# Kernel tuning notes

Measured on AMD Instinct MI355X. Metric: run time of the kernel, lower is better.

## Reference

```python
import jax, jax.numpy as jnp
import numpy as np

BATCH, SEQ = 1, 2048
D_MODEL, N_HEADS, D_HEAD = 2048, 16, 128
ROTARY_DIM = 128
N_CTX = 2048
EPS = 1e-5
IGNORE = -100000.0
ATTN_SCALE = float(np.sqrt(D_HEAD))  # use_attn_scale=True, no layer-idx scaling
ROTARY_BASE = 10000.0


def _ln_pre(x):
    # LayerNormPre: center and normalize, no learned scale/bias
    x = x - x.mean(axis=-1, keepdims=True)
    scale = jnp.sqrt((x * x).mean(axis=-1, keepdims=True) + EPS)
    return x / scale


def _sin_cos_rotary(rotary_dim, n_ctx, base=ROTARY_BASE):
    pos = jnp.arange(n_ctx, dtype=jnp.float32)
    dim = jnp.arange(rotary_dim // 2, dtype=jnp.float32)
    freq = base ** (dim / (rotary_dim / 2))
    freq = jnp.repeat(freq, 2)  # einops.repeat 'd -> (d 2)' (interleaved)
    angles = pos[:, None] / freq[None, :]  # [n_ctx, rotary_dim]
    return jnp.sin(angles), jnp.cos(angles)


def _rotate_every_two(x):
    x1 = x[..., 0::2]
    x2 = x[..., 1::2]
    return jnp.stack([-x2, x1], axis=-1).reshape(x.shape)


def _apply_rotary(x, sin, cos):
    # x: [batch, pos, head, d_head]
    n_pos = x.shape[1]
    x_rot = x[..., :ROTARY_DIM]
    x_pass = x[..., ROTARY_DIM:]
    c = cos[:n_pos][:, None, :]  # [pos, 1, rotary_dim] broadcasts over head
    s = sin[:n_pos][:, None, :]
    x_rotated = x_rot * c + _rotate_every_two(x_rot) * s
    return jnp.concatenate([x_rotated, x_pass], axis=-1)


def setup_inputs() -> dict:
    key = jax.random.key(0)
    ks = jax.random.split(key, 6)
    init_std = 0.02
    return {
        "resid_pre": jax.random.normal(ks[0], (BATCH, SEQ, D_MODEL), jnp.float32),
        "W_Q": jax.random.normal(ks[1], (N_HEADS, D_MODEL, D_HEAD), jnp.float32) * init_std,
        "W_K": jax.random.normal(ks[2], (N_HEADS, D_MODEL, D_HEAD), jnp.float32) * init_std,
        "W_V": jax.random.normal(ks[3], (N_HEADS, D_MODEL, D_HEAD), jnp.float32) * init_std,
        "W_O": jax.random.normal(ks[4], (N_HEADS, D_HEAD, D_MODEL), jnp.float32) * init_std,
        "b_Q": jnp.zeros((N_HEADS, D_HEAD), jnp.float32),
        "b_K": jnp.zeros((N_HEADS, D_HEAD), jnp.float32),
        "b_V": jnp.zeros((N_HEADS, D_HEAD), jnp.float32),
        "b_O": jnp.zeros((D_MODEL,), jnp.float32),
    }


def reference(resid_pre, W_Q, W_K, W_V, W_O, b_Q, b_K, b_V, b_O):
    sin, cos = _sin_cos_rotary(ROTARY_DIM, N_CTX)
    xn = _ln_pre(resid_pre)  # LayerNormPre applied to resid_pre for q, k, v
    q = jnp.einsum("bpd,hde->bphe", xn, W_Q) + b_Q
    k = jnp.einsum("bpd,hde->bphe", xn, W_K) + b_K
    v = jnp.einsum("bpd,hde->bphe", xn, W_V) + b_V
    q = _apply_rotary(q, sin, cos)
    k = _apply_rotary(k, sin, cos)
    # attn_scores: [batch, head, query_pos, key_pos]
    scores = jnp.einsum("bqhe,bkhe->bhqk", q, k) / ATTN_SCALE
    n_pos = resid_pre.shape[1]
    causal = jnp.tril(jnp.ones((n_pos, n_pos), dtype=bool))
    scores = jnp.where(causal, scores, jnp.float32(IGNORE))
    attn = jax.nn.softmax(scores, axis=-1)
    z = jnp.einsum("bkhe,bhqk->bqhe", v, attn)
    out = jnp.einsum("bqhe,hed->bqd", z, W_O) + b_O
    return out
```

## Files before the change

### kernel.cpp

```cpp
#include <hip/hip_runtime.h>
#include <hip/hip_bf16.h>

#define SEQ    2048
#define DM     2048
#define NH     16
#define DH     128
#define EPS    1e-5f
#define SCALE_INV 0.08838834764831845f
#define SC2LOG    0.12751744995f

typedef unsigned short u16;
typedef u16  u16x4  __attribute__((ext_vector_type(4)));
typedef u16  u16x8  __attribute__((ext_vector_type(8)));
typedef __bf16 bf16x8 __attribute__((ext_vector_type(8)));
typedef float f32x4 __attribute__((ext_vector_type(4)));

__device__ __forceinline__ u16 f2bf(float f) {
    unsigned int u = __builtin_bit_cast(unsigned int, f);
    u += 0x7fffu + ((u >> 16) & 1u);
    return (u16)(u >> 16);
}
__device__ __forceinline__ bf16x8 as_bf(u16x8 v) { return __builtin_bit_cast(bf16x8, v); }

__device__ __forceinline__ void gload16(const u16* g, u16* l) {
    __builtin_amdgcn_global_load_lds(
        (const __attribute__((address_space(1))) unsigned int*)g,
        (__attribute__((address_space(3))) unsigned int*)l, 16, 0, 0);
}

#define VMCNT(N) asm volatile("s_waitcnt vmcnt(" #N ")" ::: "memory")
#define LGKMCNT0 asm volatile("s_waitcnt lgkmcnt(0)" ::: "memory")
#define SCHEDBAR __builtin_amdgcn_sched_barrier(0)
#define BARRIER  __builtin_amdgcn_s_barrier()

__global__ void rope_kernel(float2* __restrict__ tab) {
    int i = threadIdx.x;
    int pos = blockIdx.x;
    float freq = powf(10000.f, (float)i * (1.f / 64.f));
    float ang = (float)pos / freq;
    tab[pos * 64 + i] = make_float2(sinf(ang), cosf(ang));
}

__global__ __launch_bounds__(256) void ln_kernel(const float* __restrict__ x,
                                                 u16* __restrict__ xn) {
    int row = blockIdx.x, t = threadIdx.x;
    const float* xr = x + (size_t)row * DM;
    float4 v0 = *(const float4*)(xr + t * 4);
    float4 v1 = *(const float4*)(xr + 1024 + t * 4);
    float s = v0.x + v0.y + v0.z + v0.w + v1.x + v1.y + v1.z + v1.w;
    float q = v0.x*v0.x + v0.y*v0.y + v0.z*v0.z + v0.w*v0.w
            + v1.x*v1.x + v1.y*v1.y + v1.z*v1.z + v1.w*v1.w;
    #pragma unroll
    for (int o = 32; o; o >>= 1) { s += __shfl_xor(s, o); q += __shfl_xor(q, o); }
    __shared__ float ss[4], qq[4];
    if ((t & 63) == 0) { ss[t >> 6] = s; qq[t >> 6] = q; }
    __syncthreads();
    s = ss[0] + ss[1] + ss[2] + ss[3];
    q = qq[0] + qq[1] + qq[2] + qq[3];
    float mean = s * (1.f / DM);
    float var  = q * (1.f / DM) - mean * mean;
    float rstd = rsqrtf(var + EPS);
    u16* orow = xn + (size_t)row * DM;
    u16x4 o0 = { f2bf((v0.x-mean)*rstd), f2bf((v0.y-mean)*rstd),
                 f2bf((v0.z-mean)*rstd), f2bf((v0.w-mean)*rstd) };
    u16x4 o1 = { f2bf((v1.x-mean)*rstd), f2bf((v1.y-mean)*rstd),
                 f2bf((v1.z-mean)*rstd), f2bf((v1.w-mean)*rstd) };
    *(u16x4*)(orow + t * 4) = o0;
    *(u16x4*)(orow + 1024 + t * 4) = o1;
}

__global__ __launch_bounds__(256) void transpose_qkv(const float* __restrict__ WQ,
                                                     const float* __restrict__ WK,
                                                     const float* __restrict__ WV,
                                                     u16* __restrict__ out) {
    int z = blockIdx.z, which = z >> 4, h = z & 15;
    const float* in = ((which == 0) ? WQ : (which == 1) ? WK : WV) + (size_t)h * DM * DH;
    u16* o = out + (size_t)z * DM * DH;
    int r0 = blockIdx.y * 64, c0 = blockIdx.x * 64;
    __shared__ u16 tile[64][65];
    int t = threadIdx.x;
    #pragma unroll
    for (int it = 0; it < 4; ++it) {
        int idx = t + it * 256;
        int rr = idx >> 4, cc = (idx & 15) * 4;
        float4 v = *(const float4*)(in + (size_t)(r0 + rr) * DH + c0 + cc);
        tile[rr][cc+0] = f2bf(v.x); tile[rr][cc+1] = f2bf(v.y);
        tile[rr][cc+2] = f2bf(v.z); tile[rr][cc+3] = f2bf(v.w);
    }
    __syncthreads();
    #pragma unroll
    for (int it = 0; it < 4; ++it) {
        int idx = t + it * 256;
        int oc = idx >> 4, orr = (idx & 15) * 4;
        u16x4 w = { tile[orr+0][oc], tile[orr+1][oc], tile[orr+2][oc], tile[orr+3][oc] };
        *(u16x4*)(o + (size_t)(c0 + oc) * DM + r0 + orr) = w;
    }
}

__global__ __launch_bounds__(256) void transpose_wo(const float* __restrict__ in,
                                                    u16* __restrict__ out) {
    int r0 = blockIdx.y * 64, c0 = blockIdx.x * 64;
    __shared__ u16 tile[64][65];
    int t = threadIdx.x;
    #pragma unroll
    for (int it = 0; it < 4; ++it) {
        int idx = t + it * 256;
        int rr = idx >> 4, cc = (idx & 15) * 4;
        float4 v = *(const float4*)(in + (size_t)(r0 + rr) * DM + c0 + cc);
        tile[rr][cc+0] = f2bf(v.x); tile[rr][cc+1] = f2bf(v.y);
        tile[rr][cc+2] = f2bf(v.z); tile[rr][cc+3] = f2bf(v.w);
    }
    __syncthreads();
    #pragma unroll
    for (int it = 0; it < 4; ++it) {
        int idx = t + it * 256;
        int oc = idx >> 4, orr = (idx & 15) * 4;
        u16x4 w = { tile[orr+0][oc], tile[orr+1][oc], tile[orr+2][oc], tile[orr+3][oc] };
        *(u16x4*)(out + (size_t)(c0 + oc) * DM + r0 + orr) = w;
    }
}

__global__ __launch_bounds__(512, 2) void gemm_qkv(const u16* __restrict__ Xn,
                                                   const u16* __restrict__ Wt,
                                                   const float* __restrict__ bQ,
                                                   const float* __restrict__ bK,
                                                   const float* __restrict__ bV,
                                                   const float2* __restrict__ rope,
                                                   u16* __restrict__ qkv) {
    __shared__ u16 As[2][256 * 64], Bs[2][256 * 64];
    int id = blockIdx.x;
    int swz = (id & 7) * 24 + (id >> 3);
    int bx = swz & 7, by = swz >> 3;
    int m0 = bx * 256, n0 = by * 256;

    int t = threadIdx.x, lane = t & 63, wid = t >> 6;
    int wr = wid >> 2, wc = wid & 3;
    int cl = lane & 15, g = lane >> 4;

    auto stage = [&](int buf, int kt) {
        const u16* xa = Xn + (size_t)kt * 64;
        const u16* xb = Wt + (size_t)kt * 64;
        #pragma unroll
        for (int j = 0; j < 4; ++j) {
            int idx = t + j * 512;
            int row = idx >> 3;
            int slotS = (idx & 7) ^ (row & 7);
            gload16(xa + (size_t)(m0 + row) * DM + slotS * 8, &As[buf][idx * 8]);
            gload16(xb + (size_t)(n0 + row) * DM + slotS * 8, &Bs[buf][idx * 8]);
        }
    };

    f32x4 acc[8][4] = {};
    stage(0, 0);
    VMCNT(0);
    BARRIER;

    for (int kt = 0; kt < 32; ++kt) {
        int p = kt & 1;
        bool more = (kt + 1 < 32);
        bf16x8 bfr[4][2], af[4][2];
        #pragma unroll
        for (int nj = 0; nj < 4; ++nj)
            #pragma unroll
            for (int kk = 0; kk < 2; ++kk) {
                int row = wc * 64 + nj * 16 + cl;
                int s = (kk * 4 + g) ^ (row & 7);
                bfr[nj][kk] = as_bf(*(const u16x8*)&Bs[p][row * 64 + s * 8]);
            }
        #pragma unroll
        for (int mi = 0; mi < 4; ++mi)
            #pragma unroll
            for (int kk = 0; kk < 2; ++kk) {
                int row = wr * 128 + mi * 16 + cl;
                int s = (kk * 4 + g) ^ (row & 7);
                af[mi][kk] = as_bf(*(const u16x8*)&As[p][row * 64 + s * 8]);
            }
        if (more) stage(p ^ 1, kt + 1);
        __builtin_amdgcn_s_setprio(1);
        #pragma unroll
        for (int mi = 0; mi < 4; ++mi)
            #pragma unroll
            for (int nj = 0; nj < 4; ++nj)
                #pragma unroll
                for (int kk = 0; kk < 2; ++kk)
                    acc[mi][nj] = __builtin_amdgcn_mfma_f32_16x16x32_bf16(af[mi][kk], bfr[nj][kk], acc[mi][nj], 0, 0, 0);
        __builtin_amdgcn_s_setprio(0);
        #pragma unroll
        for (int mi = 0; mi < 4; ++mi)
            #pragma unroll
            for (int kk = 0; kk < 2; ++kk) {
                int row = wr * 128 + 64 + mi * 16 + cl;
                int s = (kk * 4 + g) ^ (row & 7);
                af[mi][kk] = as_bf(*(const u16x8*)&As[p][row * 64 + s * 8]);
            }
        __builtin_amdgcn_s_setprio(1);
        #pragma unroll
        for (int mi = 0; mi < 4; ++mi)
            #pragma unroll
            for (int nj = 0; nj < 4; ++nj)
                #pragma unroll
                for (int kk = 0; kk < 2; ++kk)
                    acc[4 + mi][nj] = __builtin_amdgcn_mfma_f32_16x16x32_bf16(af[mi][kk], bfr[nj][kk], acc[4 + mi][nj], 0, 0, 0);
        __builtin_amdgcn_s_setprio(0);
        VMCNT(0);
        SCHEDBAR;
        BARRIER;
    }

    int which = n0 >> 11;
    const float* bias = (which == 0) ? bQ : (which == 1) ? bK : bV;
    #pragma unroll
    for (int i = 0; i < 8; ++i)
        #pragma unroll
        for (int nj = 0; nj < 4; ++nj) {
            int eg = n0 + wc * 64 + nj * 16 + cl;
            int h = (eg >> 7) & 15;
            int e = eg & 127;
            float bb = bias[h * DH + e];
            int p0 = m0 + wr * 128 + i * 16 + g * 4;
            if (which == 2) {
                u16* vbase = qkv + 2ll * NH * SEQ * DH + (size_t)h * DH * SEQ;
                u16x4 o = { f2bf(acc[i][nj][0] + bb), f2bf(acc[i][nj][1] + bb),
                            f2bf(acc[i][nj][2] + bb), f2bf(acc[i][nj][3] + bb) };
                *(u16x4*)(vbase + (size_t)e * SEQ + p0) = o;
            } else {
                u16* outbase = qkv + ((size_t)which * 16 + h) * SEQ * DH;
                #pragma unroll
                for (int r = 0; r < 4; ++r) {
                    int pp = p0 + r;
                    float v = acc[i][nj][r] + bb;
                    float pv = __shfl_xor(v, 1);
                    float2 sc2 = rope[pp * 64 + (e >> 1)];
                    v = (e & 1) ? (v * sc2.y + pv * sc2.x) : (v * sc2.y - pv * sc2.x);
                    outbase[(size_t)pp * DH + e] = f2bf(v);
                }
            }
        }
}

__global__ __launch_bounds__(256) void flash_kernel(const u16* __restrict__ Qg,
                                                    const u16* __restrict__ Kg,
                                                    const u16* __restrict__ Vt,
                                                    u16* __restrict__ Zg) {
    __shared__ u16 kt[64 * 128];
    __shared__ u16 vt[128 * 64];
    __shared__ unsigned pt32[4 * 16 * 32];
    int h = blockIdx.x;
    int nQ = gridDim.y;
    int q0 = (nQ - 1 - blockIdx.y) * 64;
    int t = threadIdx.x, lane = t & 63, w = t >> 6;
    int cl = lane & 15, g = lane >> 4;
    int qw0 = q0 + w * 16;
    const size_t hs = (size_t)h * SEQ;
    unsigned* ptw = pt32 + w * (16 * 32) + cl * 32;
    int swv = (cl & 7) << 1;

    bf16x8 qf[4];
    #pragma unroll
    for (int st = 0; st < 4; ++st)
        qf[st] = as_bf(*(const u16x8*)(Qg + (hs + qw0 + cl) * DH + st * 32 + g * 8));

    f32x4 acc[8] = {};
    float mrun = -3e38f, lsum = 0.f;

    u16x8 kreg[4], vreg[4];
    auto load_tile = [&](int kv0) {
        #pragma unroll
        for (int j = 0; j < 4; ++j) {
            int idx = t + j * 256;
            kreg[j] = *(const u16x8*)(Kg + (hs + kv0 + (idx >> 4)) * DH + (idx & 15) * 8);
            vreg[j] = *(const u16x8*)(Vt + ((size_t)h * DH + (idx >> 3)) * SEQ + kv0 + (idx & 7) * 8);
        }
    };
    auto store_tile = [&]() {
        #pragma unroll
        for (int j = 0; j < 4; ++j) {
            int idx = t + j * 256;
            int row = idx >> 4, slot = idx & 15;
            *(u16x8*)((char*)kt + row * 256 + ((slot ^ (row & 7)) * 16)) = kreg[j];
            int e = idx >> 3, ch = idx & 7;
            *(u16x8*)((char*)vt + e * 128 + ((ch ^ (e & 7)) * 16)) = vreg[j];
        }
    };

    load_tile(0);
    store_tile();

    for (int kv0 = 0; kv0 <= q0; kv0 += 64) {
        __syncthreads();
        bool more = (kv0 + 64 <= q0);
        if (more) load_tile(kv0 + 64);

        f32x4 sc[4] = {};
        #pragma unroll
        for (int st = 0; st < 4; ++st)
            #pragma unroll
            for (int c = 0; c < 4; ++c) {
                int row = c * 16 + cl;
                bf16x8 kf = as_bf(*(const u16x8*)((char*)kt + row * 256 + (((st * 4 + g) ^ (row & 7)) * 16)));
                sc[c] = __builtin_amdgcn_mfma_f32_16x16x32_bf16(kf, qf[st], sc[c], 0, 0, 0);
            }

        bool needmask = (kv0 + 63 > qw0);
        int qrow = qw0 + cl;
        float pf[4][4];
        float tm = -3e38f;
        #pragma unroll
        for (int c = 0; c < 4; ++c)
            #pragma unroll
            for (int r = 0; r < 4; ++r) {
                int kvq = kv0 + c * 16 + g * 4 + r;
                float sval = sc[c][r] * SC2LOG;
                if (needmask) sval = (kvq <= qrow) ? sval : -3e38f;
                pf[c][r] = sval;
                tm = fmaxf(tm, sval);
            }
        tm = fmaxf(tm, __shfl_xor(tm, 16));
        tm = fmaxf(tm, __shfl_xor(tm, 32));

        if (!__all(tm <= mrun + 12.f)) {
            float mn = fmaxf(mrun, tm);
            float alpha = exp2f(mrun - mn);
            mrun = mn;
            lsum *= alpha;
            float aR[4];
            #pragma unroll
            for (int r = 0; r < 4; ++r) aR[r] = __shfl(alpha, g * 4 + r);
            #pragma unroll
            for (int n = 0; n < 8; ++n)
                #pragma unroll
                for (int r = 0; r < 4; ++r) acc[n][r] *= aR[r];
        }
        float rs = 0.f;
        #pragma unroll
        for (int c = 0; c < 4; ++c)
            #pragma unroll
            for (int r = 0; r < 4; ++r) {
                float e2 = exp2f(pf[c][r] - mrun);
                pf[c][r] = e2;
                rs += e2;
            }
        rs += __shfl_xor(rs, 16);
        rs += __shfl_xor(rs, 32);
        lsum += rs;

        #pragma unroll
        for (int c = 0; c < 4; ++c) {
            unsigned lo = (unsigned)f2bf(pf[c][0]) | ((unsigned)f2bf(pf[c][1]) << 16);
            unsigned hi = (unsigned)f2bf(pf[c][2]) | ((unsigned)f2bf(pf[c][3]) << 16);
            int u = (c * 4 + g) ^ swv;
            *(unsigned long long*)(ptw + u * 2) =
                (unsigned long long)lo | ((unsigned long long)hi << 32);
        }
        bf16x8 pa[2];
        #pragma unroll
        for (int ks = 0; ks < 2; ++ks)
            pa[ks] = as_bf(*(const u16x8*)(ptw + ((ks * 8 + g * 2) ^ swv) * 2));

        #pragma unroll
        for (int n = 0; n < 8; ++n)
            #pragma unroll
            for (int ks = 0; ks < 2; ++ks) {
                int e = n * 16 + cl;
                bf16x8 vf = as_bf(*(const u16x8*)((char*)vt + e * 128 + (((ks * 4 + g) ^ (e & 7)) * 16)));
                acc[n] = __builtin_amdgcn_mfma_f32_16x16x32_bf16(pa[ks], vf, acc[n], 0, 0, 0);
            }

        if (!more) break;
        __syncthreads();
        store_tile();
    }

    float inv = 1.0f / lsum;
    float invR[4];
    #pragma unroll
    for (int r = 0; r < 4; ++r) invR[r] = __shfl(inv, g * 4 + r);
    #pragma unroll
    for (int n = 0; n < 8; ++n)
        #pragma unroll
        for (int r = 0; r < 4; ++r) {
            int q = qw0 + g * 4 + r;
            Zg[(hs + q) * DH + n * 16 + cl] = f2bf(acc[n][r] * invR[r]);
        }
}

__global__ __launch_bounds__(256) void gemm_out(const u16* __restrict__ Z,
                                                const u16* __restrict__ Wot,
                                                const float* __restrict__ bO,
                                                float* __restrict__ out) {
    __shared__ u16 As[2 * 128 * 32], Bs[2 * 128 * 32];
    int m0 = blockIdx.x * 128, n0 = blockIdx.y * 128;
    int t = threadIdx.x, lane = t & 63, w = t >> 6;
    int wr = w >> 1, wc = w & 1;
    int cl = lane & 15, g = lane >> 4;
    int swz = (cl >> 1) & 3;

    auto stage = [&](int buf, int k0) {
        u16* Ab = As + buf * (128 * 32);
        u16* Bb = Bs + buf * (128 * 32);
        int hh = k0 >> 7, e0 = k0 & 127;
        #pragma unroll
        for (int j = 0; j < 2; ++j) {
            int idx = t + j * 256;
            int row = idx >> 2, slot = idx & 3;
            int slotS = slot ^ ((row >> 1) & 3);
            gload16(Z + ((size_t)hh * SEQ + m0 + row) * DH + e0 + slotS * 8, Ab + idx * 8);
            gload16(Wot + (size_t)(n0 + row) * DM + k0 + slotS * 8, Bb + idx * 8);
        }
    };

    f32x4 acc[4][4] = {};
    stage(0, 0);
    int cur = 0;
    for (int k0 = 0; k0 < DM; k0 += 32) {
        bool more = (k0 + 32 < DM);
        if (more) {
            stage(cur ^ 1, k0 + 32);
            VMCNT(4);
        } else {
            VMCNT(0);
        }
        SCHEDBAR;
        BARRIER;
        const u16* Ac = As + cur * (128 * 32);
        const u16* Bc = Bs + cur * (128 * 32);
        bf16x8 af[4], bfr[4];
        #pragma unroll
        for (int i = 0; i < 4; ++i)
            af[i] = as_bf(*(const u16x8*)&Ac[(wr*64 + i*16 + cl) * 32 + (g ^ swz) * 8]);
        #pragma unroll
        for (int j = 0; j < 4; ++j)
            bfr[j] = as_bf(*(const u16x8*)&Bc[(wc*64 + j*16 + cl) * 32 + (g ^ swz) * 8]);
        #pragma unroll
        for (int i = 0; i < 4; ++i)
            #pragma unroll
            for (int j = 0; j < 4; ++j)
                acc[i][j] = __builtin_amdgcn_mfma_f32_16x16x32_bf16(af[i], bfr[j], acc[i][j], 0, 0, 0);
        LGKMCNT0;
        SCHEDBAR;
        BARRIER;
        cur ^= 1;
    }
    #pragma unroll
    for (int i = 0; i < 4; ++i)
        #pragma unroll
        for (int j = 0; j < 4; ++j) {
            int col = n0 + wc * 64 + j * 16 + cl;
            float bb = bO[col];
            #pragma unroll
            for (int r = 0; r < 4; ++r) {
                int p = m0 + wr * 64 + i * 16 + g * 4 + r;
                out[(size_t)p * DM + col] = acc[i][j][r] + bb;
            }
        }
}

extern "C" void kernel_launch(void* const* d_in, const int* in_sizes, int n_in,
                              void* d_out, int out_size, void* d_ws, size_t ws_size,
                              hipStream_t stream) {
    const float* resid = (const float*)d_in[0];
    const float* WQ = (const float*)d_in[1];
    const float* WK = (const float*)d_in[2];
    const float* WV = (const float*)d_in[3];
    const float* WO = (const float*)d_in[4];
    const float* bQ = (const float*)d_in[5];
    const float* bK = (const float*)d_in[6];
    const float* bV = (const float*)d_in[7];
    const float* bO = (const float*)d_in[8];
    float* out = (float*)d_out;
    char* ws = (char*)d_ws;

    float2* rope = (float2*)(ws);
    u16* xn   = (u16*)(ws + (1ll  << 20));
    u16* Wt   = (u16*)(ws + (9ll  << 20));
    u16* Wot  = (u16*)(ws + (33ll << 20));
    u16* qkv  = (u16*)(ws + (41ll << 20));
    u16* z    = (u16*)(ws + (65ll << 20));

    rope_kernel<<<SEQ, 64, 0, stream>>>(rope);
    ln_kernel<<<SEQ, 256, 0, stream>>>(resid, xn);

    transpose_qkv<<<dim3(2, 32, 48), 256, 0, stream>>>(WQ, WK, WV, Wt);
    transpose_wo<<<dim3(32, 32, 1), 256, 0, stream>>>(WO, Wot);

    gemm_qkv<<<192, 512, 0, stream>>>(xn, Wt, bQ, bK, bV, rope, qkv);

    const u16* Qg = qkv;
    const u16* Kg = qkv + 1ll * NH * SEQ * DH;
    const u16* Vt = qkv + 2ll * NH * SEQ * DH;
    flash_kernel<<<dim3(NH, SEQ / 64), 256, 0, stream>>>(Qg, Kg, Vt, z);

    gemm_out<<<dim3(16, 16), 256, 0, stream>>>(z, Wot, bO, out);
}
```

Measured before the change: 203.3 us.

## Split causal attention KV range into chunks with partial outputs and merge kernel

Each query tile's causal KV range is split into chunks of at most 8 KV tiles, and each chunk is processed by its own workgroup. That gives 80 workgroups per head instead of 32, each with bounded work, which removes the long tail from the largest query tiles. Multi-chunk tiles write unnormalized bf16 partial outputs plus running max and sum to workspace, and a new merge kernel combines them with log-sum-exp weights. MFMA sections are also wrapped in s_setprio to raise wave priority. The cost is an extra launch, extra global traffic for the partials, and bf16 rounding of partial accumulators. The partial buffer reuses workspace that earlier stages already consumed.

```diff
diff --git a/kernel.cpp b/kernel.cpp
--- a/kernel.cpp
+++ b/kernel.cpp
@@ -19,6 +19,9 @@
     unsigned int u = __builtin_bit_cast(unsigned int, f);
     u += 0x7fffu + ((u >> 16) & 1u);
     return (u16)(u >> 16);
+}
+__device__ __forceinline__ float bf2f(u16 v) {
+    return __builtin_bit_cast(float, (unsigned)v << 16);
 }
 __device__ __forceinline__ bf16x8 as_bf(u16x8 v) { return __builtin_bit_cast(bf16x8, v); }
 
@@ -238,16 +241,34 @@
         }
 }
 
+__device__ __forceinline__ int part_prefix(int j) {
+    return (j < 16) ? 2 * (j - 8) : (j < 24 ? 16 + 3 * (j - 16) : 40 + 4 * (j - 24));
+}
+
 __global__ __launch_bounds__(256) void flash_kernel(const u16* __restrict__ Qg,
                                                     const u16* __restrict__ Kg,
                                                     const u16* __restrict__ Vt,
-                                                    u16* __restrict__ Zg) {
+                                                    u16* __restrict__ Zg,
+                                                    u16* __restrict__ pO,
+                                                    float2* __restrict__ ml) {
     __shared__ u16 kt[64 * 128];
     __shared__ u16 vt[128 * 64];
     __shared__ unsigned pt32[4 * 16 * 32];
     int h = blockIdx.x;
-    int nQ = gridDim.y;
-    int q0 = (nQ - 1 - blockIdx.y) * 64;
+    int rem = blockIdx.y;
+    int j = 31, c = 0;
+    #pragma unroll 1
+    for (int jj = 31; jj >= 0; --jj) {
+        int ncj = (jj >> 3) + 1;
+        if (rem < ncj) { j = jj; c = rem; break; }
+        rem -= ncj;
+    }
+    int q0 = j * 64;
+    int nc = (j >> 3) + 1;
+    bool multi = (nc > 1);
+    int kt0 = c * 8;
+    int kt1 = min(j, c * 8 + 7);
+
     int t = threadIdx.x, lane = t & 63, w = t >> 6;
     int cl = lane & 15, g = lane >> 4;
     int qw0 = q0 + w * 16;
@@ -266,53 +287,56 @@
     u16x8 kreg[4], vreg[4];
     auto load_tile = [&](int kv0) {
         #pragma unroll
-        for (int j = 0; j < 4; ++j) {
-            int idx = t + j * 256;
-            kreg[j] = *(const u16x8*)(Kg + (hs + kv0 + (idx >> 4)) * DH + (idx & 15) * 8);
-            vreg[j] = *(const u16x8*)(Vt + ((size_t)h * DH + (idx >> 3)) * SEQ + kv0 + (idx & 7) * 8);
+        for (int jj = 0; jj < 4; ++jj) {
+            int idx = t + jj * 256;
+            kreg[jj] = *(const u16x8*)(Kg + (hs + kv0 + (idx >> 4)) * DH + (idx & 15) * 8);
+            vreg[jj] = *(const u16x8*)(Vt + ((size_t)h * DH + (idx >> 3)) * SEQ + kv0 + (idx & 7) * 8);
         }
     };
     auto store_tile = [&]() {
         #pragma unroll
-        for (int j = 0; j < 4; ++j) {
-            int idx = t + j * 256;
+        for (int jj = 0; jj < 4; ++jj) {
+            int idx = t + jj * 256;
             int row = idx >> 4, slot = idx & 15;
-            *(u16x8*)((char*)kt + row * 256 + ((slot ^ (row & 7)) * 16)) = kreg[j];
+            *(u16x8*)((char*)kt + row * 256 + ((slot ^ (row & 7)) * 16)) = kreg[jj];
             int e = idx >> 3, ch = idx & 7;
-            *(u16x8*)((char*)vt + e * 128 + ((ch ^ (e & 7)) * 16)) = vreg[j];
+            *(u16x8*)((char*)vt + e * 128 + ((ch ^ (e & 7)) * 16)) = vreg[jj];
         }
     };
 
-    load_tile(0);
+    int kvbeg = kt0 * 64, kvend = kt1 * 64;
+    load_tile(kvbeg);
     store_tile();
 
-    for (int kv0 = 0; kv0 <= q0; kv0 += 64) {
+    for (int kv0 = kvbeg; kv0 <= kvend; kv0 += 64) {
         __syncthreads();
-        bool more = (kv0 + 64 <= q0);
+        bool more = (kv0 + 64 <= kvend);
         if (more) load_tile(kv0 + 64);
 
         f32x4 sc[4] = {};
+        __builtin_amdgcn_s_setprio(1);
         #pragma unroll
         for (int st = 0; st < 4; ++st)
             #pragma unroll
-            for (int c = 0; c < 4; ++c) {
-                int row = c * 16 + cl;
+            for (int cc = 0; cc < 4; ++cc) {
+                int row = cc * 16 + cl;
                 bf16x8 kf = as_bf(*(const u16x8*)((char*)kt + row * 256 + (((st * 4 + g) ^ (row & 7)) * 16)));
-                sc[c] = __builtin_amdgcn_mfma_f32_16x16x32_bf16(kf, qf[st], sc[c], 0, 0, 0);
-            }
+                sc[cc] = __builtin_amdgcn_mfma_f32_16x16x32_bf16(kf, qf[st], sc[cc], 0, 0, 0);
+            }
+        __builtin_amdgcn_s_setprio(0);
 
         bool needmask = (kv0 + 63 > qw0);
         int qrow = qw0 + cl;
         float pf[4][4];
         float tm = -3e38f;
         #pragma unroll
-        for (int c = 0; c < 4; ++c)
+        for (int cc = 0; cc < 4; ++cc)
             #pragma unroll
             for (int r = 0; r < 4; ++r) {
-                int kvq = kv0 + c * 16 + g * 4 + r;
-                float sval = sc[c][r] * SC2LOG;
+                int kvq = kv0 + cc * 16 + g * 4 + r;
+                float sval = sc[cc][r] * SC2LOG;
                 if (needmask) sval = (kvq <= qrow) ? sval : -3e38f;
-                pf[c][r] = sval;
+                pf[cc][r] = sval;
                 tm = fmaxf(tm, sval);
             }
         tm = fmaxf(tm, __shfl_xor(tm, 16));
@@ -333,11 +357,11 @@
         }
         float rs = 0.f;
         #pragma unroll
-        for (int c = 0; c < 4; ++c)
+        for (int cc = 0; cc < 4; ++cc)
             #pragma unroll
             for (int r = 0; r < 4; ++r) {
-                float e2 = exp2f(pf[c][r] - mrun);
-                pf[c][r] = e2;
+                float e2 = exp2f(pf[cc][r] - mrun);
+                pf[cc][r] = e2;
                 rs += e2;
             }
         rs += __shfl_xor(rs, 16);
@@ -345,10 +369,10 @@
         lsum += rs;
 
         #pragma unroll
-        for (int c = 0; c < 4; ++c) {
-            unsigned lo = (unsigned)f2bf(pf[c][0]) | ((unsigned)f2bf(pf[c][1]) << 16);
-            unsigned hi = (unsigned)f2bf(pf[c][2]) | ((unsigned)f2bf(pf[c][3]) << 16);
-            int u = (c * 4 + g) ^ swv;
+        for (int cc = 0; cc < 4; ++cc) {
+            unsigned lo = (unsigned)f2bf(pf[cc][0]) | ((unsigned)f2bf(pf[cc][1]) << 16);
+            unsigned hi = (unsigned)f2bf(pf[cc][2]) | ((unsigned)f2bf(pf[cc][3]) << 16);
+            int u = (cc * 4 + g) ^ swv;
             *(unsigned long long*)(ptw + u * 2) =
                 (unsigned long long)lo | ((unsigned long long)hi << 32);
         }
@@ -357,6 +381,7 @@
         for (int ks = 0; ks < 2; ++ks)
             pa[ks] = as_bf(*(const u16x8*)(ptw + ((ks * 8 + g * 2) ^ swv) * 2));
 
+        __builtin_amdgcn_s_setprio(1);
         #pragma unroll
         for (int n = 0; n < 8; ++n)
             #pragma unroll
@@ -365,23 +390,81 @@
                 bf16x8 vf = as_bf(*(const u16x8*)((char*)vt + e * 128 + (((ks * 4 + g) ^ (e & 7)) * 16)));
                 acc[n] = __builtin_amdgcn_mfma_f32_16x16x32_bf16(pa[ks], vf, acc[n], 0, 0, 0);
             }
+        __builtin_amdgcn_s_setprio(0);
 
         if (!more) break;
         __syncthreads();
         store_tile();
     }
 
-    float inv = 1.0f / lsum;
-    float invR[4];
-    #pragma unroll
-    for (int r = 0; r < 4; ++r) invR[r] = __shfl(inv, g * 4 + r);
-    #pragma unroll
-    for (int n = 0; n < 8; ++n)
-        #pragma unroll
-        for (int r = 0; r < 4; ++r) {
-            int q = qw0 + g * 4 + r;
-            Zg[(hs + q) * DH + n * 16 + cl] = f2bf(acc[n][r] * invR[r]);
-        }
+    if (multi) {
+        int pidx = h * 72 + part_prefix(j) + c;
+        if (lane < 16) ml[(size_t)pidx * 64 + w * 16 + cl] = make_float2(mrun, lsum);
+        u16* po = pO + (size_t)pidx * (64 * 128);
+        #pragma unroll
+        for (int n = 0; n < 8; ++n)
+            #pragma unroll
+            for (int r = 0; r < 4; ++r)
+                po[(w * 16 + g * 4 + r) * 128 + n * 16 + cl] = f2bf(acc[n][r]);
+    } else {
+        float inv = 1.0f / lsum;
+        float invR[4];
+        #pragma unroll
+        for (int r = 0; r < 4; ++r) invR[r] = __shfl(inv, g * 4 + r);
+        #pragma unroll
+        for (int n = 0; n < 8; ++n)
+            #pragma unroll
+            for (int r = 0; r < 4; ++r) {
+                int q = qw0 + g * 4 + r;
+                Zg[(hs + q) * DH + n * 16 + cl] = f2bf(acc[n][r] * invR[r]);
+            }
+    }
+}
+
+__global__ __launch_bounds__(256) void merge_kernel(const u16* __restrict__ pO,
+                                                    const float2* __restrict__ ml,
+                                                    u16* __restrict__ Zg) {
+    int h = blockIdx.x;
+    int j = blockIdx.y + 8;
+    int nc = (j >> 3) + 1;
+    int pbase = h * 72 + part_prefix(j);
+    int t = threadIdx.x;
+    int row = t >> 2;
+    int c0 = (t & 3) * 32;
+
+    float mv[4], lv[4];
+    float M = -3e38f;
+    #pragma unroll
+    for (int i = 0; i < 4; ++i) {
+        int ii = (i < nc) ? i : 0;
+        float2 mli = ml[(size_t)(pbase + ii) * 64 + row];
+        mv[i] = mli.x; lv[i] = mli.y;
+        if (i < nc) M = fmaxf(M, mli.x);
+    }
+    float wgt[4];
+    float L = 0.f;
+    #pragma unroll
+    for (int i = 0; i < 4; ++i) {
+        wgt[i] = (i < nc) ? exp2f(mv[i] - M) : 0.f;
+        L += wgt[i] * lv[i];
+    }
+    float invL = 1.f / L;
+
+    #pragma unroll
+    for (int ccc = 0; ccc < 32; ccc += 8) {
+        float o[8] = {};
+        #pragma unroll
+        for (int i = 0; i < 4; ++i) {
+            int ii = (i < nc) ? i : 0;
+            u16x8 v = *(const u16x8*)(pO + ((size_t)(pbase + ii) * 64 + row) * 128 + c0 + ccc);
+            #pragma unroll
+            for (int k = 0; k < 8; ++k) o[k] += wgt[i] * bf2f(v[k]);
+        }
+        u16x8 zv;
+        #pragma unroll
+        for (int k = 0; k < 8; ++k) zv[k] = f2bf(o[k] * invL);
+        *(u16x8*)(Zg + ((size_t)h * SEQ + j * 64 + row) * DH + c0 + ccc) = zv;
+    }
 }
 
 __global__ __launch_bounds__(256) void gemm_out(const u16* __restrict__ Z,
@@ -476,6 +559,8 @@
     u16* Wot  = (u16*)(ws + (33ll << 20));
     u16* qkv  = (u16*)(ws + (41ll << 20));
     u16* z    = (u16*)(ws + (65ll << 20));
+    u16* pO   = (u16*)(ws);
+    float2* ml = (float2*)(ws + (20ll << 20));
 
     rope_kernel<<<SEQ, 64, 0, stream>>>(rope);
     ln_kernel<<<SEQ, 256, 0, stream>>>(resid, xn);
@@ -488,7 +573,8 @@
     const u16* Qg = qkv;
     const u16* Kg = qkv + 1ll * NH * SEQ * DH;
     const u16* Vt = qkv + 2ll * NH * SEQ * DH;
-    flash_kernel<<<dim3(NH, SEQ / 64), 256, 0, stream>>>(Qg, Kg, Vt, z);
+    flash_kernel<<<dim3(NH, 80), 256, 0, stream>>>(Qg, Kg, Vt, z, pO, ml);
+    merge_kernel<<<dim3(NH, 24), 256, 0, stream>>>(pO, ml, z);
 
     gemm_out<<<dim3(16, 16), 256, 0, stream>>>(z, Wot, bO, out);
 }
```

New measurement: 201.0 us. About the same (-1.2%).
